# Kernel tuning notes

Measured on AMD Instinct MI355X. Metric: run time of the kernel, lower is better.

## Reference

```python
import jax, jax.numpy as jnp
import numpy as np

IN_F, OUT_F, STYLE_F = 512, 512, 256
B, N = 2, 131072


def setup_inputs() -> dict:
    key = jax.random.key(0)
    ks = jax.random.split(key, 5)
    x = jax.random.normal(ks[0], (B, N, IN_F), dtype=jnp.float32)
    z = jax.random.normal(ks[1], (B, STYLE_F), dtype=jnp.float32)
    # Parameters, initialized as in the torch module
    weight = jax.random.normal(ks[2], (OUT_F, IN_F), dtype=jnp.float32) / np.sqrt(IN_F)
    weight_alpha = jax.random.normal(ks[3], (IN_F, STYLE_F), dtype=jnp.float32) / np.sqrt(STYLE_F)
    bias_alpha = jnp.ones((IN_F,), dtype=jnp.float32)
    weight_beta = jax.random.normal(ks[4], (OUT_F, STYLE_F), dtype=jnp.float32) / np.sqrt(STYLE_F)
    bias_beta = jnp.zeros((OUT_F,), dtype=jnp.float32)
    return {"x": x, "z": z, "weight": weight, "weight_alpha": weight_alpha,
            "bias_alpha": bias_alpha, "weight_beta": weight_beta, "bias_beta": bias_beta}


def reference(x, z, weight, weight_alpha, bias_alpha, weight_beta, bias_beta):
    # ModLinear forward with bias=False, mod_bias=True, output_mode=True.
    # alpha: [B, in] style-derived input-channel modulation
    alpha = z @ weight_alpha.T + bias_alpha
    # beta: [B, out] style-derived output bias (output_mode=True)
    beta = z @ weight_beta.T + bias_beta
    # torch: w_mod = weight[None] * alpha[:, None, :]; out = baddbmm(beta, x, w_mod^T)
    # Equivalent fused form: (x * alpha) @ weight.T + beta, avoiding the [B,out,in] tensor.
    out = jnp.einsum('bni,oi->bno', x * alpha[:, None, :], weight) + beta[:, None, :]
    return out
```

## Files before the change

kernel.cpp:

```cpp
#include <hip/hip_runtime.h>

typedef __attribute__((ext_vector_type(4))) float f32x4;
typedef __attribute__((ext_vector_type(8))) short s16x8;

#define IN_F 512
#define OUT_F 512
#define STYLE_F 256

typedef __attribute__((address_space(1))) const void gvoid;
typedef __attribute__((address_space(3))) void svoid;

__device__ __forceinline__ unsigned short f2bf(float f) {
    unsigned int u = __builtin_bit_cast(unsigned int, f);
    u += 0x7FFFu + ((u >> 16) & 1u);
    return (unsigned short)(u >> 16);
}

__device__ __forceinline__ s16x8 cvt8(f32x4 a, f32x4 b) {
    union { unsigned int w[4]; s16x8 v; } u;
    asm("v_cvt_pk_bf16_f32 %0, %1, %2" : "=v"(u.w[0]) : "v"(a[0]), "v"(a[1]));
    asm("v_cvt_pk_bf16_f32 %0, %1, %2" : "=v"(u.w[1]) : "v"(a[2]), "v"(a[3]));
    asm("v_cvt_pk_bf16_f32 %0, %1, %2" : "=v"(u.w[2]) : "v"(b[0]), "v"(b[1]));
    asm("v_cvt_pk_bf16_f32 %0, %1, %2" : "=v"(u.w[3]) : "v"(b[2]), "v"(b[3]));
    return u.v;
}

__global__ __launch_bounds__(256) void prep1_kernel(
    const float* __restrict__ z,
    const float* __restrict__ w_alpha,
    const float* __restrict__ b_alpha,
    const float* __restrict__ w_beta,
    const float* __restrict__ b_beta,
    float* __restrict__ alpha,
    float* __restrict__ beta)
{
    int gid = blockIdx.x * 256 + threadIdx.x;
    if (gid >= 2048) return;
    int t = gid & 1023;
    int b = t >> 9;
    int i = t & 511;
    const float* zr = z + b * STYLE_F;
    const float* wr = (gid < 1024 ? w_alpha : w_beta) + i * STYLE_F;
    float acc = 0.f;
    #pragma unroll 4
    for (int kk = 0; kk < STYLE_F; kk += 4) {
        float4 zv = *reinterpret_cast<const float4*>(zr + kk);
        float4 vv = *reinterpret_cast<const float4*>(wr + kk);
        acc += zv.x * vv.x + zv.y * vv.y + zv.z * vv.z + zv.w * vv.w;
    }
    if (gid < 1024) alpha[t] = acc + b_alpha[i];
    else            beta[t]  = acc + b_beta[i];
}

__global__ __launch_bounds__(256) void prep2_kernel(
    const float* __restrict__ weight,
    const float* __restrict__ alpha,
    unsigned short* __restrict__ wfragB)
{
    int gid = blockIdx.x * 256 + threadIdx.x;
    int b = gid >> 16;
    int f = (gid & 65535) << 2;
    int e0 = f & 7;
    int l  = (f >> 3) & 63;
    int nf = (f >> 9) & 31;
    int ks = f >> 14;
    int n  = nf * 16 + (l & 15);
    int k  = ks * 32 + ((l >> 4) << 3) + e0;
    float4 wv = *reinterpret_cast<const float4*>(weight + n * IN_F + k);
    float4 av = *reinterpret_cast<const float4*>(alpha + b * IN_F + k);
    ushort4 o;
    o.x = f2bf(wv.x * av.x); o.y = f2bf(wv.y * av.y);
    o.z = f2bf(wv.z * av.z); o.w = f2bf(wv.w * av.w);
    *reinterpret_cast<ushort4*>(wfragB + b * 262144 + f) = o;
}

__global__ __launch_bounds__(512, 2) void modlin_kernel(
    const float* __restrict__ x,
    const unsigned short* __restrict__ wfragB,
    const float* __restrict__ beta,
    float* __restrict__ out)
{
    __shared__ __align__(16) char lds[2 * 32768];

    const int tid = threadIdx.x;
    const int blk = blockIdx.x;
    const int b   = blk >> 7;

    const int l  = tid & 63;
    const int w  = tid >> 6;
    const int wm = w >> 2;
    const int wn = w & 3;
    const int fr = l & 15;
    const int fq = l >> 4;
    const int wvbase = w << 10;

    const int dr = tid >> 4;
    const int du = (tid & 8) | ((tid & 7) ^ (dr & 7));
    const float* xp0 = x + (size_t)(blk * 1024 +  0 + dr) * IN_F + du * 4;
    const float* xp1 = x + (size_t)(blk * 1024 + 32 + dr) * IN_F + du * 4;
    const float* xp2 = x + (size_t)(blk * 1024 + 64 + dr) * IN_F + du * 4;
    const float* xp3 = x + (size_t)(blk * 1024 + 96 + dr) * IN_F + du * 4;

    int va[8];
    #pragma unroll
    for (int mf = 0; mf < 4; ++mf) {
        int R = wm * 64 + mf * 16 + fr;
        va[mf * 2 + 0] = R * 256 + ((((fq * 2) + 0) ^ (fr & 7)) << 4);
        va[mf * 2 + 1] = R * 256 + ((((fq * 2) + 1) ^ (fr & 7)) << 4);
    }

    const char* bbp = (const char*)wfragB + (size_t)b * 524288;
    const unsigned vobase = (unsigned)(wn * 8192 + l * 16);

    float bv[8];
    #pragma unroll
    for (int nf = 0; nf < 8; ++nf)
        bv[nf] = beta[b * OUT_F + wn * 128 + nf * 16 + fr];

    f32x4 acc[4][8];
    s16x8 bb[8], bc[8];

    #define ISSUE4(NB)                                                         \
        do {                                                                   \
            __builtin_amdgcn_global_load_lds((gvoid*)xp0,                      \
                (svoid*)(lds + (NB) * 32768 + wvbase +     0), 16, 0, 0);      \
            __builtin_amdgcn_global_load_lds((gvoid*)xp1,                      \
                (svoid*)(lds + (NB) * 32768 + wvbase +  8192), 16, 0, 0);      \
            __builtin_amdgcn_global_load_lds((gvoid*)xp2,                      \
                (svoid*)(lds + (NB) * 32768 + wvbase + 16384), 16, 0, 0);      \
            __builtin_amdgcn_global_load_lds((gvoid*)xp3,                      \
                (svoid*)(lds + (NB) * 32768 + wvbase + 24576), 16, 0, 0);      \
        } while (0)

    #define LOADB8(dst, KS)                                                    \
        do {                                                                   \
            unsigned voA_ = vobase + (unsigned)(KS) * 32768u;                  \
            unsigned voB_ = voA_ + 4096u;                                      \
            _Pragma("unroll")                                                  \
            for (int nf_ = 0; nf_ < 4; ++nf_) {                                \
                asm volatile("global_load_dwordx4 %0, %1, %2 offset:%3"        \
                    : "=v"(dst[nf_])     : "v"(voA_), "s"(bbp),                \
                      "n"(nf_ * 1024) : "memory");                             \
                asm volatile("global_load_dwordx4 %0, %1, %2 offset:%3"        \
                    : "=v"(dst[nf_ + 4]) : "v"(voB_), "s"(bbp),                \
                      "n"(nf_ * 1024) : "memory");                             \
            }                                                                  \
        } while (0)

    #define READA(dst, BUF, S)                                                 \
        do {                                                                   \
            _Pragma("unroll")                                                  \
            for (int mf_ = 0; mf_ < 4; ++mf_) {                                \
                f32x4 r0_ = *(const f32x4*)(lds + (BUF) * 32768 + (S) * 128    \
                                            + va[mf_ * 2 + 0]);                \
                f32x4 r1_ = *(const f32x4*)(lds + (BUF) * 32768 + (S) * 128    \
                                            + va[mf_ * 2 + 1]);                \
                dst[mf_] = cvt8(r0_, r1_);                                     \
            }                                                                  \
        } while (0)

    #define MFMA32(A4, B8)                                                     \
        do {                                                                   \
            _Pragma("unroll")                                                  \
            for (int nf_ = 0; nf_ < 8; ++nf_)                                  \
                _Pragma("unroll")                                              \
                for (int mf_ = 0; mf_ < 4; ++mf_)                              \
                    acc[mf_][nf_] = __builtin_amdgcn_mfma_f32_16x16x32_bf16(   \
                        A4[mf_], B8[nf_], acc[mf_][nf_], 0, 0, 0);             \
        } while (0)

    ISSUE4(0);
    xp0 += 64; xp1 += 64; xp2 += 64; xp3 += 64;
    asm volatile("s_waitcnt vmcnt(0)" ::: "memory");
    __builtin_amdgcn_sched_barrier(0);

    for (int j = 0; j < 8; ++j) {
        #pragma unroll
        for (int mf = 0; mf < 4; ++mf)
            #pragma unroll
            for (int nf = 0; nf < 8; ++nf)
                acc[mf][nf] = (f32x4){0.f, 0.f, 0.f, 0.f};

        #pragma unroll
        for (int t = 0; t < 8; ++t) {
            const int buf  = t & 1;
            const int nbuf = buf ^ 1;
            __builtin_amdgcn_s_barrier();
            __builtin_amdgcn_sched_barrier(0);

            LOADB8(bb, t * 2);
            LOADB8(bc, t * 2 + 1);
            const bool last = (t == 7) && (j == 7);
            if (t < 7) {
                ISSUE4(nbuf);
                xp0 += 64; xp1 += 64; xp2 += 64; xp3 += 64;
            } else if (j < 7) {
                xp0 += 65024; xp1 += 65024; xp2 += 65024; xp3 += 65024;
                ISSUE4(nbuf);
                xp0 += 64; xp1 += 64; xp2 += 64; xp3 += 64;
            }

            s16x8 a0[4];
            READA(a0, buf, 0);
            if (!last) asm volatile("s_waitcnt vmcnt(12)" ::: "memory");
            else       asm volatile("s_waitcnt vmcnt(8)"  ::: "memory");
            __builtin_amdgcn_sched_barrier(0);
            MFMA32(a0, bb);

            s16x8 a1[4];
            READA(a1, buf, 1);
            if (!last) asm volatile("s_waitcnt vmcnt(4)" ::: "memory");
            else       asm volatile("s_waitcnt vmcnt(0)" ::: "memory");
            __builtin_amdgcn_sched_barrier(0);
            MFMA32(a1, bc);

            if (!last) {
                asm volatile("s_waitcnt vmcnt(0)" ::: "memory");
                __builtin_amdgcn_sched_barrier(0);
            }
        }

        float* op = out + (size_t)(blk * 1024 + j * 128 + wm * 64 + fq * 4) * OUT_F
                        + wn * 128 + fr;
        #pragma unroll
        for (int nf = 0; nf < 8; ++nf)
            #pragma unroll
            for (int mf = 0; mf < 4; ++mf) {
                float* p = op + (mf * 16) * OUT_F + nf * 16;
                p[0 * OUT_F] = acc[mf][nf][0] + bv[nf];
                p[1 * OUT_F] = acc[mf][nf][1] + bv[nf];
                p[2 * OUT_F] = acc[mf][nf][2] + bv[nf];
                p[3 * OUT_F] = acc[mf][nf][3] + bv[nf];
            }
    }

    #undef ISSUE4
    #undef LOADB8
    #undef READA
    #undef MFMA32
}

extern "C" void kernel_launch(void* const* d_in, const int* in_sizes, int n_in,
                              void* d_out, int out_size, void* d_ws, size_t ws_size,
                              hipStream_t stream)
{
    const float* x       = (const float*)d_in[0];
    const float* z       = (const float*)d_in[1];
    const float* weight  = (const float*)d_in[2];
    const float* w_alpha = (const float*)d_in[3];
    const float* b_alpha = (const float*)d_in[4];
    const float* w_beta  = (const float*)d_in[5];
    const float* b_beta  = (const float*)d_in[6];
    float* out = (float*)d_out;

    unsigned short* wfragB = (unsigned short*)d_ws;
    float* alpha = (float*)((char*)d_ws + 1048576);
    float* beta  = alpha + 2 * IN_F;

    prep1_kernel<<<8, 256, 0, stream>>>(z, w_alpha, b_alpha, w_beta, b_beta,
                                        alpha, beta);
    prep2_kernel<<<512, 256, 0, stream>>>(weight, alpha, wfragB);
    modlin_kernel<<<256, 512, 0, stream>>>(x, wfragB, beta, out);
}
```

Baseline: 389.8 us.

## Triple-buffer x tiles in LDS and stage output stores through LDS for vectorized writes

Moves the x-tile pipeline from double to triple buffering with two tiles in flight, dropping the trailing full vmcnt(0) wait so global loads overlap more with MFMA work. The epilogue now transposes accumulators through a per-wave LDS staging area so each lane writes contiguous float4 rows instead of scalar strided stores. LDS use rises to 128 KB per block, which with launch_bounds(512,2) may cut occupancy to one block per CU. The per-wave staging has no explicit sync between the LDS write and read, which relies on wave-level ordering.

```diff
diff --git a/kernel.cpp b/kernel.cpp
--- a/kernel.cpp
+++ b/kernel.cpp
@@ -80,7 +80,7 @@
     const float* __restrict__ beta,
     float* __restrict__ out)
 {
-    __shared__ __align__(16) char lds[2 * 32768];
+    __shared__ __align__(16) char lds[131072];
 
     const int tid = threadIdx.x;
     const int blk = blockIdx.x;
@@ -117,19 +117,21 @@
     for (int nf = 0; nf < 8; ++nf)
         bv[nf] = beta[b * OUT_F + wn * 128 + nf * 16 + fr];
 
+    float* stgf = (float*)(lds + 98304 + w * 4096);
+
     f32x4 acc[4][8];
     s16x8 bb[8], bc[8];
 
-    #define ISSUE4(NB)                                                         \
+    #define ISSUE4(WRB)                                                        \
         do {                                                                   \
             __builtin_amdgcn_global_load_lds((gvoid*)xp0,                      \
-                (svoid*)(lds + (NB) * 32768 + wvbase +     0), 16, 0, 0);      \
+                (svoid*)(lds + (WRB) + wvbase +     0), 16, 0, 0);             \
             __builtin_amdgcn_global_load_lds((gvoid*)xp1,                      \
-                (svoid*)(lds + (NB) * 32768 + wvbase +  8192), 16, 0, 0);      \
+                (svoid*)(lds + (WRB) + wvbase +  8192), 16, 0, 0);             \
             __builtin_amdgcn_global_load_lds((gvoid*)xp2,                      \
-                (svoid*)(lds + (NB) * 32768 + wvbase + 16384), 16, 0, 0);      \
+                (svoid*)(lds + (WRB) + wvbase + 16384), 16, 0, 0);             \
             __builtin_amdgcn_global_load_lds((gvoid*)xp3,                      \
-                (svoid*)(lds + (NB) * 32768 + wvbase + 24576), 16, 0, 0);      \
+                (svoid*)(lds + (WRB) + wvbase + 24576), 16, 0, 0);             \
         } while (0)
 
     #define LOADB8(dst, KS)                                                    \
@@ -147,13 +149,13 @@
             }                                                                  \
         } while (0)
 
-    #define READA(dst, BUF, S)                                                 \
+    #define READA(dst, RDB, S)                                                 \
         do {                                                                   \
             _Pragma("unroll")                                                  \
             for (int mf_ = 0; mf_ < 4; ++mf_) {                                \
-                f32x4 r0_ = *(const f32x4*)(lds + (BUF) * 32768 + (S) * 128    \
+                f32x4 r0_ = *(const f32x4*)(lds + (RDB) + (S) * 128            \
                                             + va[mf_ * 2 + 0]);                \
-                f32x4 r1_ = *(const f32x4*)(lds + (BUF) * 32768 + (S) * 128    \
+                f32x4 r1_ = *(const f32x4*)(lds + (RDB) + (S) * 128            \
                                             + va[mf_ * 2 + 1]);                \
                 dst[mf_] = cvt8(r0_, r1_);                                     \
             }                                                                  \
@@ -169,9 +171,44 @@
                         A4[mf_], B8[nf_], acc[mf_][nf_], 0, 0, 0);             \
         } while (0)
 
-    ISSUE4(0);
+    #define STEP(RDB, WRB, T)                                                  \
+        do {                                                                   \
+            __builtin_amdgcn_s_barrier();                                      \
+            __builtin_amdgcn_sched_barrier(0);                                 \
+            LOADB8(bb, (T) * 2);                                               \
+            LOADB8(bc, (T) * 2 + 1);                                           \
+            bool issue_ = ((T) < 6) || (j < 7);                                \
+            if ((T) == 6 && j < 7) {                                           \
+                xp0 += 65024; xp1 += 65024; xp2 += 65024; xp3 += 65024;        \
+            }                                                                  \
+            if (issue_) {                                                      \
+                ISSUE4(WRB);                                                   \
+                xp0 += 64; xp1 += 64; xp2 += 64; xp3 += 64;                    \
+            }                                                                  \
+            s16x8 a0_[4];                                                      \
+            READA(a0_, RDB, 0);                                                \
+            if ((T) < 6 || j < 7)                                              \
+                asm volatile("s_waitcnt vmcnt(12)" ::: "memory");              \
+            else                                                               \
+                asm volatile("s_waitcnt vmcnt(8)" ::: "memory");               \
+            __builtin_amdgcn_sched_barrier(0);                                 \
+            MFMA32(a0_, bb);                                                   \
+            s16x8 a1_[4];                                                      \
+            READA(a1_, RDB, 1);                                                \
+            if ((T) < 6 || j < 7)                                              \
+                asm volatile("s_waitcnt vmcnt(4)" ::: "memory");               \
+            else                                                               \
+                asm volatile("s_waitcnt vmcnt(0)" ::: "memory");               \
+            __builtin_amdgcn_sched_barrier(0);                                 \
+            MFMA32(a1_, bc);                                                   \
+        } while (0)
+
+    int b0 = 0, b1 = 32768, b2 = 65536;
+    ISSUE4(b0);
     xp0 += 64; xp1 += 64; xp2 += 64; xp3 += 64;
-    asm volatile("s_waitcnt vmcnt(0)" ::: "memory");
+    ISSUE4(b1);
+    xp0 += 64; xp1 += 64; xp2 += 64; xp3 += 64;
+    asm volatile("s_waitcnt vmcnt(4)" ::: "memory");
     __builtin_amdgcn_sched_barrier(0);
 
     for (int j = 0; j < 8; ++j) {
@@ -181,63 +218,45 @@
             for (int nf = 0; nf < 8; ++nf)
                 acc[mf][nf] = (f32x4){0.f, 0.f, 0.f, 0.f};
 
+        STEP(b0, b2, 0);
+        STEP(b1, b0, 1);
+        STEP(b2, b1, 2);
+        STEP(b0, b2, 3);
+        STEP(b1, b0, 4);
+        STEP(b2, b1, 5);
+        STEP(b0, b2, 6);
+        STEP(b1, b0, 7);
+        { int tp = b0; b0 = b2; b2 = b1; b1 = tp; }
+
+        const long long orow = (long long)(blk * 1024 + j * 128 + wm * 64);
         #pragma unroll
-        for (int t = 0; t < 8; ++t) {
-            const int buf  = t & 1;
-            const int nbuf = buf ^ 1;
-            __builtin_amdgcn_s_barrier();
-            __builtin_amdgcn_sched_barrier(0);
-
-            LOADB8(bb, t * 2);
-            LOADB8(bc, t * 2 + 1);
-            const bool last = (t == 7) && (j == 7);
-            if (t < 7) {
-                ISSUE4(nbuf);
-                xp0 += 64; xp1 += 64; xp2 += 64; xp3 += 64;
-            } else if (j < 7) {
-                xp0 += 65024; xp1 += 65024; xp2 += 65024; xp3 += 65024;
-                ISSUE4(nbuf);
-                xp0 += 64; xp1 += 64; xp2 += 64; xp3 += 64;
-            }
-
-            s16x8 a0[4];
-            READA(a0, buf, 0);
-            if (!last) asm volatile("s_waitcnt vmcnt(12)" ::: "memory");
-            else       asm volatile("s_waitcnt vmcnt(8)"  ::: "memory");
-            __builtin_amdgcn_sched_barrier(0);
-            MFMA32(a0, bb);
-
-            s16x8 a1[4];
-            READA(a1, buf, 1);
-            if (!last) asm volatile("s_waitcnt vmcnt(4)" ::: "memory");
-            else       asm volatile("s_waitcnt vmcnt(0)" ::: "memory");
-            __builtin_amdgcn_sched_barrier(0);
-            MFMA32(a1, bc);
-
-            if (!last) {
-                asm volatile("s_waitcnt vmcnt(0)" ::: "memory");
-                __builtin_amdgcn_sched_barrier(0);
+        for (int mf = 0; mf < 4; ++mf) {
+            #pragma unroll
+            for (int half = 0; half < 2; ++half) {
+                #pragma unroll
+                for (int nf4 = 0; nf4 < 4; ++nf4) {
+                    int nf = half * 4 + nf4;
+                    #pragma unroll
+                    for (int e = 0; e < 4; ++e)
+                        stgf[(fq * 4 + e) * 64 + nf4 * 16 + fr] =
+                            acc[mf][nf][e] + bv[nf];
+                }
+                #pragma unroll
+                for (int s = 0; s < 4; ++s) {
+                    f32x4 v = *(const f32x4*)(stgf + (s * 4 + fq) * 64 + fr * 4);
+                    float* p = out + (orow + mf * 16 + s * 4 + fq) * OUT_F
+                                   + wn * 128 + half * 64 + fr * 4;
+                    *(f32x4*)p = v;
+                }
             }
         }
-
-        float* op = out + (size_t)(blk * 1024 + j * 128 + wm * 64 + fq * 4) * OUT_F
-                        + wn * 128 + fr;
-        #pragma unroll
-        for (int nf = 0; nf < 8; ++nf)
-            #pragma unroll
-            for (int mf = 0; mf < 4; ++mf) {
-                float* p = op + (mf * 16) * OUT_F + nf * 16;
-                p[0 * OUT_F] = acc[mf][nf][0] + bv[nf];
-                p[1 * OUT_F] = acc[mf][nf][1] + bv[nf];
-                p[2 * OUT_F] = acc[mf][nf][2] + bv[nf];
-                p[3 * OUT_F] = acc[mf][nf][3] + bv[nf];
-            }
     }
 
     #undef ISSUE4
     #undef LOADB8
     #undef READA
     #undef MFMA32
+    #undef STEP
 }
 
 extern "C" void kernel_launch(void* const* d_in, const int* in_sizes, int n_in,
```

Result: no change. 393.7 us (+1.0%).
